# Optimization experiments

Hardware: AMD Instinct MI355X
Metric: run time of the kernel (lower is better)

## Reference

```python
import jax, jax.numpy as jnp
import numpy as np

MODES1 = 32
MODES2 = 32


def _dct1_last(x):
    # Unnormalized DCT-I along last axis via rfft of even-symmetric extension.
    # For length N input, extension [x0..x_{N-1}, x_{N-2}..x_1] has length 2(N-1);
    # rfft yields N real coefficients == scipy.fftpack.dct(x, type=1).
    ext = jnp.concatenate([x, x[..., -2:0:-1]], axis=-1)
    return jnp.fft.rfft(ext, axis=-1).real.astype(x.dtype)


def _dct1_2d(x):
    # DCT-I along last two axes (separable). scipy idct type-1 (unnormalized)
    # is identical to dct type-1, so this serves as both dctn and idctn.
    x = _dct1_last(x)
    x = jnp.swapaxes(x, -1, -2)
    x = _dct1_last(x)
    return jnp.swapaxes(x, -1, -2)


def setup_inputs() -> dict:
    key = jax.random.key(0)
    k1, k2, k3 = jax.random.split(key, 3)
    B, Cin, Cout, H, W = 8, 64, 64, 256, 256
    scale = 1.0 / (Cin * Cout)
    x = jax.random.normal(k1, (B, Cin, H, W), dtype=jnp.float32)
    weights1 = scale * jax.random.uniform(k2, (Cin, Cout, MODES1, MODES2), dtype=jnp.float32)
    weights2 = scale * jax.random.uniform(k3, (Cin, Cout, MODES1, MODES2), dtype=jnp.float32)
    return {"x": x, "weights1": weights1, "weights2": weights2}


def reference(x, weights1, weights2):
    B, Cin, H, W = x.shape
    Cout = weights1.shape[1]
    Wh = W // 2 + 1  # width of truncated spectral tensor (torch used cfloat, imag==0)
    m1, m2 = MODES1, MODES2

    x_dct = _dct1_2d(x)  # [B, Cin, H, W]

    low = jnp.einsum('bixy,ioxy->boxy', x_dct[:, :, :m1, :m2], weights1)
    high = jnp.einsum('bixy,ioxy->boxy', x_dct[:, :, -m1:, :m2], weights2)

    out_ft = jnp.zeros((B, Cout, H, Wh), dtype=x.dtype)
    out_ft = out_ft.at[:, :, :m1, :m2].set(low)
    out_ft = out_ft.at[:, :, H - m1:, :m2].set(high)

    # idctn(..., type=1, shape=(H, W)) zero-pads the last axis from Wh to W,
    # then applies unnormalized IDCT-I == DCT-I along axes 2,3.
    out_full = jnp.pad(out_ft, ((0, 0), (0, 0), (0, 0), (0, W - Wh)))
    return _dct1_2d(out_full)
```

## Files before the change

kernel.cpp:

```cpp
#include <hip/hip_runtime.h>
#include <math.h>

#define OFF_AT  0
#define OFF_BMT 16384
#define OFF_CMT 24576
#define OFF_DMT 40960
#define OFF_T   49152
#define OFF_Y   4243456
#define OFF_Z   5292032

__device__ __forceinline__ float cosT(int p) {
    int r = p % 510;
    if (r > 255) r = 510 - r;
    return cosf((float)r * (3.14159265358979323846f / 255.0f));
}

__global__ __launch_bounds__(256) void init_basis(float* __restrict__ ws) {
    int idx = blockIdx.x * 256 + threadIdx.x;
    if (idx < 16384) {
        int h = idx >> 6, r = idx & 63;
        int k1 = (r < 32) ? r : r + 192;
        float we = (h == 0 || h == 255) ? 1.f : 2.f;
        ws[OFF_AT + idx] = we * cosT(k1 * h);
    } else if (idx < 24576) {
        int j = idx - 16384; int w = j >> 5, y = j & 31;
        float we = (w == 0 || w == 255) ? 1.f : 2.f;
        ws[OFF_BMT + j] = we * cosT(y * w);
    } else if (idx < 40960) {
        int j = idx - 24576; int r = j >> 8, h = j & 255;
        int k1 = (r < 32) ? r : r + 192;
        float wsl = (r == 0 || r == 63) ? 1.f : 2.f;
        ws[OFF_CMT + j] = wsl * cosT(k1 * h);
    } else if (idx < 49152) {
        int j = idx - 40960; int y = j >> 8, w = j & 255;
        float wy = (y == 0) ? 1.f : 2.f;
        ws[OFF_DMT + j] = wy * cosT(y * w);
    }
}

__global__ __launch_bounds__(256) void fwd1_kernel(const float* __restrict__ x,
                                                   const float* __restrict__ ws,
                                                   float* __restrict__ T1) {
    __shared__ float xs[128 * 33];
    __shared__ float bs[32 * 32];
    const int t = threadIdx.x;
    const int bi = blockIdx.x >> 1;
    const int rt = (blockIdx.x & 1) * 128;
    const float* xp = x + (size_t)bi * 65536 + (size_t)rt * 256;
    const int l = t & 63;
    const int y8 = (t >> 6) * 8;
    const int colv = (t & 7) * 4;
    const int rbase = t >> 3;

    float acc0[8], acc1[8];
#pragma unroll
    for (int yy = 0; yy < 8; ++yy) { acc0[yy] = 0.f; acc1[yy] = 0.f; }

    for (int c = 0; c < 8; ++c) {
#pragma unroll
        for (int r = 0; r < 4; ++r) {
            int row = r * 32 + rbase;
            float4 v = *(const float4*)(xp + row * 256 + c * 32 + colv);
            float* dst = &xs[row * 33 + colv];
            dst[0] = v.x; dst[1] = v.y; dst[2] = v.z; dst[3] = v.w;
        }
        {
            int wloc = t >> 3;
            int y4 = (t & 7) * 4;
            *(float4*)&bs[wloc * 32 + y4] =
                *(const float4*)(ws + OFF_BMT + (c * 32 + wloc) * 32 + y4);
        }
        __syncthreads();
#pragma unroll 8
        for (int w = 0; w < 32; ++w) {
            float xv0 = xs[l * 33 + w];
            float xv1 = xs[(l + 64) * 33 + w];
            float4 b0 = *(float4*)&bs[w * 32 + y8];
            float4 b1 = *(float4*)&bs[w * 32 + y8 + 4];
            float bv[8] = {b0.x, b0.y, b0.z, b0.w, b1.x, b1.y, b1.z, b1.w};
#pragma unroll
            for (int yy = 0; yy < 8; ++yy) {
                acc0[yy] += xv0 * bv[yy];
                acc1[yy] += xv1 * bv[yy];
            }
        }
        __syncthreads();
    }
    float* Tp = T1 + (size_t)bi * 8192 + (size_t)(rt + l) * 32 + y8;
    *(float4*)Tp       = make_float4(acc0[0], acc0[1], acc0[2], acc0[3]);
    *(float4*)(Tp + 4) = make_float4(acc0[4], acc0[5], acc0[6], acc0[7]);
    Tp += 64 * 32;
    *(float4*)Tp       = make_float4(acc1[0], acc1[1], acc1[2], acc1[3]);
    *(float4*)(Tp + 4) = make_float4(acc1[4], acc1[5], acc1[6], acc1[7]);
}

__global__ __launch_bounds__(256) void fwd2_kernel(const float* __restrict__ ws,
                                                   const float* __restrict__ T1,
                                                   float* __restrict__ Y) {
    __shared__ float t1s[8192];
    const int t = threadIdx.x;
    const int bi = blockIdx.x;
    const float* Tp = T1 + (size_t)bi * 8192;
#pragma unroll
    for (int k = 0; k < 8; ++k)
        *(float4*)&t1s[k * 1024 + t * 4] = *(const float4*)(Tp + k * 1024 + t * 4);
    __syncthreads();
    const int l = t & 63;
    const int y8 = (t >> 6) * 8;
    float acc[8];
#pragma unroll
    for (int yy = 0; yy < 8; ++yy) acc[yy] = 0.f;
    const float* At = ws + OFF_AT + l;
#pragma unroll 4
    for (int h = 0; h < 256; ++h) {
        float av = At[h * 64];
        float4 t0 = *(float4*)&t1s[h * 32 + y8];
        float4 t1v = *(float4*)&t1s[h * 32 + y8 + 4];
        acc[0] += av * t0.x;  acc[1] += av * t0.y;
        acc[2] += av * t0.z;  acc[3] += av * t0.w;
        acc[4] += av * t1v.x; acc[5] += av * t1v.y;
        acc[6] += av * t1v.z; acc[7] += av * t1v.w;
    }
    float* Yp = Y + (size_t)bi * 2048 + l * 32 + y8;
    *(float4*)Yp       = make_float4(acc[0], acc[1], acc[2], acc[3]);
    *(float4*)(Yp + 4) = make_float4(acc[4], acc[5], acc[6], acc[7]);
}

__global__ __launch_bounds__(256) void mix_kernel(const float* __restrict__ w1,
                                                  const float* __restrict__ w2,
                                                  const float* __restrict__ Yv,
                                                  float* __restrict__ Z) {
    const int xp = blockIdx.x & 63;
    const int o0 = (blockIdx.x >> 6) * 16;
    const int t = threadIdx.x;
    const int yh = t & 15;
    const int oo = t >> 4;
    const int o = o0 + oo;
    const int y = yh * 2;

    const float* Wbase = (xp < 32) ? (w1 + xp * 32) : (w2 + (xp - 32) * 32);
    Wbase += o * 1024 + y;
    const float* Yb = Yv + xp * 32 + y;

    float acc[8][2];
#pragma unroll
    for (int b = 0; b < 8; ++b) { acc[b][0] = 0.f; acc[b][1] = 0.f; }

    for (int i = 0; i < 64; ++i) {
        float2 wv = *(const float2*)(Wbase + i * 65536);
#pragma unroll
        for (int b = 0; b < 8; ++b) {
            float2 yv = *(const float2*)(Yb + (b * 64 + i) * 2048);
            acc[b][0] += yv.x * wv.x;
            acc[b][1] += yv.y * wv.y;
        }
    }
#pragma unroll
    for (int b = 0; b < 8; ++b) {
        float2 r; r.x = acc[b][0]; r.y = acc[b][1];
        *(float2*)(Z + (size_t)(b * 64 + o) * 2048 + xp * 32 + y) = r;
    }
}

__global__ __launch_bounds__(256) void inv1_kernel(const float* __restrict__ ws,
                                                   const float* __restrict__ Zv,
                                                   float* __restrict__ T2) {
    __shared__ float zs[2048];
    const int t = threadIdx.x;
    const int bo = blockIdx.x >> 1;
    const int ht = (blockIdx.x & 1) * 128;
    const float* Zp = Zv + (size_t)bo * 2048;
    *(float4*)&zs[t * 8]     = *(const float4*)(Zp + t * 8);
    *(float4*)&zs[t * 8 + 4] = *(const float4*)(Zp + t * 8 + 4);
    __syncthreads();
    const int l = t & 63;
    const int y8 = (t >> 6) * 8;
    float acc0[8], acc1[8];
#pragma unroll
    for (int yy = 0; yy < 8; ++yy) { acc0[yy] = 0.f; acc1[yy] = 0.f; }
    const float* Cm = ws + OFF_CMT + ht + l;
#pragma unroll 4
    for (int r = 0; r < 64; ++r) {
        float a0 = Cm[r * 256];
        float a1 = Cm[r * 256 + 64];
        float4 z0 = *(float4*)&zs[r * 32 + y8];
        float4 z1 = *(float4*)&zs[r * 32 + y8 + 4];
        float zv[8] = {z0.x, z0.y, z0.z, z0.w, z1.x, z1.y, z1.z, z1.w};
#pragma unroll
        for (int yy = 0; yy < 8; ++yy) {
            acc0[yy] += a0 * zv[yy];
            acc1[yy] += a1 * zv[yy];
        }
    }
    float* Tp = T2 + (size_t)bo * 8192 + (size_t)y8 * 256 + ht + l;
#pragma unroll
    for (int j = 0; j < 8; ++j) {
        Tp[j * 256]      = acc0[j];
        Tp[j * 256 + 64] = acc1[j];
    }
}

__global__ __launch_bounds__(256) void inv2_kernel(const float* __restrict__ ws,
                                                   const float* __restrict__ T2,
                                                   float* __restrict__ out) {
    __shared__ float t2s[32 * 68];
    const int t = threadIdx.x;
    const int bo = blockIdx.x >> 2;
    const int ht = (blockIdx.x & 3) * 64;
    const float* Tp = T2 + (size_t)bo * 8192 + ht;
    {
        int y = t >> 3;
        int c8 = (t & 7) * 8;
        *(float4*)&t2s[y * 68 + c8]     = *(const float4*)(Tp + y * 256 + c8);
        *(float4*)&t2s[y * 68 + c8 + 4] = *(const float4*)(Tp + y * 256 + c8 + 4);
    }
    __syncthreads();
    const int h8 = (t >> 5) * 8;
    const int w8 = (t & 31) * 8;
    const float* Dm = ws + OFF_DMT + w8;
    float a2[8][8];
#pragma unroll
    for (int i = 0; i < 8; ++i)
#pragma unroll
        for (int w = 0; w < 8; ++w) a2[i][w] = 0.f;
#pragma unroll 4
    for (int y = 0; y < 32; ++y) {
        float4 ta = *(float4*)&t2s[y * 68 + h8];
        float4 tb = *(float4*)&t2s[y * 68 + h8 + 4];
        float4 da = *(const float4*)(Dm + y * 256);
        float4 db = *(const float4*)(Dm + y * 256 + 4);
        float tv[8] = {ta.x, ta.y, ta.z, ta.w, tb.x, tb.y, tb.z, tb.w};
        float dv[8] = {da.x, da.y, da.z, da.w, db.x, db.y, db.z, db.w};
#pragma unroll
        for (int i = 0; i < 8; ++i)
#pragma unroll
            for (int w = 0; w < 8; ++w)
                a2[i][w] += tv[i] * dv[w];
    }
    float* op = out + (size_t)bo * 65536 + (size_t)(ht + h8) * 256 + w8;
#pragma unroll
    for (int i = 0; i < 8; ++i) {
        *(float4*)(op + i * 256)     = make_float4(a2[i][0], a2[i][1], a2[i][2], a2[i][3]);
        *(float4*)(op + i * 256 + 4) = make_float4(a2[i][4], a2[i][5], a2[i][6], a2[i][7]);
    }
}

extern "C" void kernel_launch(void* const* d_in, const int* in_sizes, int n_in,
                              void* d_out, int out_size, void* d_ws, size_t ws_size,
                              hipStream_t stream) {
    const float* x  = (const float*)d_in[0];
    const float* w1 = (const float*)d_in[1];
    const float* w2 = (const float*)d_in[2];
    float* out = (float*)d_out;
    float* ws  = (float*)d_ws;

    hipLaunchKernelGGL(init_basis, dim3(192), dim3(256), 0, stream, ws);
    hipLaunchKernelGGL(fwd1_kernel, dim3(1024), dim3(256), 0, stream, x, ws, ws + OFF_T);
    hipLaunchKernelGGL(fwd2_kernel, dim3(512), dim3(256), 0, stream, ws, ws + OFF_T, ws + OFF_Y);
    hipLaunchKernelGGL(mix_kernel, dim3(256), dim3(256), 0, stream, w1, w2,
                       ws + OFF_Y, ws + OFF_Z);
    hipLaunchKernelGGL(inv1_kernel, dim3(1024), dim3(256), 0, stream, ws, ws + OFF_Z, ws + OFF_T);
    hipLaunchKernelGGL(inv2_kernel, dim3(2048), dim3(256), 0, stream, ws, ws + OFF_T, out);
}
```

Before: 347.9 us.

## Restructure fwd1 to stream x rows from global, and spread mix over more blocks

After: 362.6 us. 1.04x slower.

```diff
diff --git a/kernel.cpp b/kernel.cpp
--- a/kernel.cpp
+++ b/kernel.cpp
@@ -41,57 +41,50 @@
 __global__ __launch_bounds__(256) void fwd1_kernel(const float* __restrict__ x,
                                                    const float* __restrict__ ws,
                                                    float* __restrict__ T1) {
-    __shared__ float xs[128 * 33];
-    __shared__ float bs[32 * 32];
+    __shared__ float bs[8192];
     const int t = threadIdx.x;
     const int bi = blockIdx.x >> 1;
-    const int rt = (blockIdx.x & 1) * 128;
-    const float* xp = x + (size_t)bi * 65536 + (size_t)rt * 256;
-    const int l = t & 63;
-    const int y8 = (t >> 6) * 8;
-    const int colv = (t & 7) * 4;
-    const int rbase = t >> 3;
-
-    float acc0[8], acc1[8];
-#pragma unroll
-    for (int yy = 0; yy < 8; ++yy) { acc0[yy] = 0.f; acc1[yy] = 0.f; }
-
-    for (int c = 0; c < 8; ++c) {
-#pragma unroll
-        for (int r = 0; r < 4; ++r) {
-            int row = r * 32 + rbase;
-            float4 v = *(const float4*)(xp + row * 256 + c * 32 + colv);
-            float* dst = &xs[row * 33 + colv];
-            dst[0] = v.x; dst[1] = v.y; dst[2] = v.z; dst[3] = v.w;
-        }
-        {
-            int wloc = t >> 3;
-            int y4 = (t & 7) * 4;
-            *(float4*)&bs[wloc * 32 + y4] =
-                *(const float4*)(ws + OFF_BMT + (c * 32 + wloc) * 32 + y4);
-        }
-        __syncthreads();
-#pragma unroll 8
-        for (int w = 0; w < 32; ++w) {
-            float xv0 = xs[l * 33 + w];
-            float xv1 = xs[(l + 64) * 33 + w];
-            float4 b0 = *(float4*)&bs[w * 32 + y8];
-            float4 b1 = *(float4*)&bs[w * 32 + y8 + 4];
+    const int rbase = (blockIdx.x & 1) * 128;
+    {
+        const float* src = ws + OFF_BMT;
+#pragma unroll
+        for (int k = 0; k < 8; ++k)
+            *(float4*)&bs[k * 1024 + t * 4] = *(const float4*)(src + k * 1024 + t * 4);
+    }
+    __syncthreads();
+
+    const int r0 = rbase + (t >> 6) * 32 + (t & 15) * 2;
+    const int y8 = ((t >> 4) & 3) * 8;
+    const float* xr = x + (size_t)bi * 65536 + (size_t)r0 * 256;
+
+    float acc[2][8];
+#pragma unroll
+    for (int j = 0; j < 2; ++j)
+#pragma unroll
+        for (int yy = 0; yy < 8; ++yy) acc[j][yy] = 0.f;
+
+    for (int w = 0; w < 256; w += 4) {
+        float4 xv0 = *(const float4*)(xr + w);
+        float4 xv1 = *(const float4*)(xr + 256 + w);
+        float xa[2][4] = {{xv0.x, xv0.y, xv0.z, xv0.w}, {xv1.x, xv1.y, xv1.z, xv1.w}};
+#pragma unroll
+        for (int k = 0; k < 4; ++k) {
+            float4 b0 = *(float4*)&bs[(w + k) * 32 + y8];
+            float4 b1 = *(float4*)&bs[(w + k) * 32 + y8 + 4];
             float bv[8] = {b0.x, b0.y, b0.z, b0.w, b1.x, b1.y, b1.z, b1.w};
 #pragma unroll
             for (int yy = 0; yy < 8; ++yy) {
-                acc0[yy] += xv0 * bv[yy];
-                acc1[yy] += xv1 * bv[yy];
+                acc[0][yy] += xa[0][k] * bv[yy];
+                acc[1][yy] += xa[1][k] * bv[yy];
             }
         }
-        __syncthreads();
-    }
-    float* Tp = T1 + (size_t)bi * 8192 + (size_t)(rt + l) * 32 + y8;
-    *(float4*)Tp       = make_float4(acc0[0], acc0[1], acc0[2], acc0[3]);
-    *(float4*)(Tp + 4) = make_float4(acc0[4], acc0[5], acc0[6], acc0[7]);
-    Tp += 64 * 32;
-    *(float4*)Tp       = make_float4(acc1[0], acc1[1], acc1[2], acc1[3]);
-    *(float4*)(Tp + 4) = make_float4(acc1[4], acc1[5], acc1[6], acc1[7]);
+    }
+    float* Tp = T1 + (size_t)bi * 8192 + (size_t)r0 * 32 + y8;
+#pragma unroll
+    for (int j = 0; j < 2; ++j) {
+        *(float4*)(Tp + j * 32)     = make_float4(acc[j][0], acc[j][1], acc[j][2], acc[j][3]);
+        *(float4*)(Tp + j * 32 + 4) = make_float4(acc[j][4], acc[j][5], acc[j][6], acc[j][7]);
+    }
 }
 
 __global__ __launch_bounds__(256) void fwd2_kernel(const float* __restrict__ ws,
@@ -111,7 +104,7 @@
 #pragma unroll
     for (int yy = 0; yy < 8; ++yy) acc[yy] = 0.f;
     const float* At = ws + OFF_AT + l;
-#pragma unroll 4
+#pragma unroll 8
     for (int h = 0; h < 256; ++h) {
         float av = At[h * 64];
         float4 t0 = *(float4*)&t1s[h * 32 + y8];
@@ -131,35 +124,28 @@
                                                   const float* __restrict__ Yv,
                                                   float* __restrict__ Z) {
     const int xp = blockIdx.x & 63;
-    const int o0 = (blockIdx.x >> 6) * 16;
-    const int t = threadIdx.x;
-    const int yh = t & 15;
-    const int oo = t >> 4;
-    const int o = o0 + oo;
-    const int y = yh * 2;
-
-    const float* Wbase = (xp < 32) ? (w1 + xp * 32) : (w2 + (xp - 32) * 32);
-    Wbase += o * 1024 + y;
-    const float* Yb = Yv + xp * 32 + y;
-
-    float acc[8][2];
-#pragma unroll
-    for (int b = 0; b < 8; ++b) { acc[b][0] = 0.f; acc[b][1] = 0.f; }
-
+    const int og = blockIdx.x >> 6;
+    const int t = threadIdx.x;
+    const int o = og * 4 + (t >> 6);
+    const int y = (t & 15) * 2;
+    const int bh = (t >> 4) & 3;
+
+    const float* Wb = ((xp < 32) ? (w1 + xp * 32) : (w2 + (xp - 32) * 32)) + o * 1024 + y;
+    const float* Y0 = Yv + (size_t)(bh * 64) * 2048 + xp * 32 + y;
+    const float* Y1 = Y0 + (size_t)4 * 64 * 2048;
+
+    float a0x = 0.f, a0y = 0.f, a1x = 0.f, a1y = 0.f;
+#pragma unroll 4
     for (int i = 0; i < 64; ++i) {
-        float2 wv = *(const float2*)(Wbase + i * 65536);
-#pragma unroll
-        for (int b = 0; b < 8; ++b) {
-            float2 yv = *(const float2*)(Yb + (b * 64 + i) * 2048);
-            acc[b][0] += yv.x * wv.x;
-            acc[b][1] += yv.y * wv.y;
-        }
-    }
-#pragma unroll
-    for (int b = 0; b < 8; ++b) {
-        float2 r; r.x = acc[b][0]; r.y = acc[b][1];
-        *(float2*)(Z + (size_t)(b * 64 + o) * 2048 + xp * 32 + y) = r;
-    }
+        float2 wv = *(const float2*)(Wb + (size_t)i * 65536);
+        float2 v0 = *(const float2*)(Y0 + (size_t)i * 2048);
+        float2 v1 = *(const float2*)(Y1 + (size_t)i * 2048);
+        a0x += v0.x * wv.x; a0y += v0.y * wv.y;
+        a1x += v1.x * wv.x; a1y += v1.y * wv.y;
+    }
+    float* Zp = Z + (size_t)(bh * 64 + o) * 2048 + xp * 32 + y;
+    *(float2*)Zp = make_float2(a0x, a0y);
+    *(float2*)(Zp + (size_t)4 * 64 * 2048) = make_float2(a1x, a1y);
 }
 
 __global__ __launch_bounds__(256) void inv1_kernel(const float* __restrict__ ws,
@@ -257,7 +243,7 @@
     hipLaunchKernelGGL(init_basis, dim3(192), dim3(256), 0, stream, ws);
     hipLaunchKernelGGL(fwd1_kernel, dim3(1024), dim3(256), 0, stream, x, ws, ws + OFF_T);
     hipLaunchKernelGGL(fwd2_kernel, dim3(512), dim3(256), 0, stream, ws, ws + OFF_T, ws + OFF_Y);
-    hipLaunchKernelGGL(mix_kernel, dim3(256), dim3(256), 0, stream, w1, w2,
+    hipLaunchKernelGGL(mix_kernel, dim3(1024), dim3(256), 0, stream, w1, w2,
                        ws + OFF_Y, ws + OFF_Z);
     hipLaunchKernelGGL(inv1_kernel, dim3(1024), dim3(256), 0, stream, ws, ws + OFF_Z, ws + OFF_T);
     hipLaunchKernelGGL(inv2_kernel, dim3(2048), dim3(256), 0, stream, ws, ws + OFF_T, out);
```
